# Kernel optimization log

Measured on AMD Instinct MI355X. Metric: run time of the kernel, lower is better.

Reference implementation:

```python
import jax, jax.numpy as jnp
import numpy as np

N_NODES = 65536
N_GRAPHS = 32
NODES_PER_GRAPH = 2048
N_EDGES = 1048576
F_IN, H1, H2, OUT = 16, 64, 64, 12


def gcn_conv(x, src, dst, W, b, num_nodes):
    """PyG GCNConv: out = D^{-1/2} (A+I) D^{-1/2} X W + b."""
    loop = jnp.arange(num_nodes, dtype=src.dtype)
    s = jnp.concatenate([src, loop])  # sources incl. self-loops
    d = jnp.concatenate([dst, loop])  # targets incl. self-loops
    deg = jax.ops.segment_sum(jnp.ones_like(d, dtype=x.dtype), d, num_segments=num_nodes)
    dinv = jnp.where(deg > 0, jax.lax.rsqrt(deg), 0.0)
    norm = dinv[s] * dinv[d]  # [E+N]
    h = x @ W  # [N, H]
    msg = h[s] * norm[:, None]  # [E+N, H] -- dominant memory traffic
    return jax.ops.segment_sum(msg, d, num_segments=num_nodes) + b


def setup_inputs() -> dict:
    key = jax.random.key(0)
    k = jax.random.split(key, 8)
    x = jax.random.normal(k[0], (N_NODES, F_IN), dtype=jnp.float32)
    edge_index = jax.random.randint(k[1], (2, N_EDGES), 0, N_NODES, dtype=jnp.int32)
    batch = jnp.repeat(jnp.arange(N_GRAPHS, dtype=jnp.int32), NODES_PER_GRAPH)
    s1 = 1.0 / np.sqrt(F_IN)
    s2 = 1.0 / np.sqrt(H1)
    s3 = 1.0 / np.sqrt(H2 * NODES_PER_GRAPH)
    W1 = jax.random.uniform(k[2], (F_IN, H1), jnp.float32, -s1, s1)
    b1 = jnp.zeros((H1,), jnp.float32)
    W2 = jax.random.uniform(k[3], (H1, H2), jnp.float32, -s2, s2)
    b2 = jnp.zeros((H2,), jnp.float32)
    Wfc = jax.random.uniform(k[4], (H2 * NODES_PER_GRAPH, OUT), jnp.float32, -s3, s3)
    bfc = jax.random.uniform(k[5], (OUT,), jnp.float32, -s3, s3)
    return {"x": x, "edge_index": edge_index, "batch": batch,
            "W1": W1, "b1": b1, "W2": W2, "b2": b2, "Wfc": Wfc, "bfc": bfc}


def reference(x, edge_index, batch, W1, b1, W2, b2, Wfc, bfc):
    src, dst = edge_index[0], edge_index[1]
    h = gcn_conv(x, src, dst, W1, b1, N_NODES)
    h = jnp.tanh(h)  # act1 (dropout rate 0 -> identity)
    h = gcn_conv(h, src, dst, W2, b2, N_NODES)
    h = jnp.tanh(h)  # act2
    # batch is sorted with exactly NODES_PER_GRAPH nodes per graph, so the
    # per-graph masked concat is a reshape: [G, P*H2]
    h_concat = h.reshape(N_GRAPHS, NODES_PER_GRAPH * H2)
    return h_concat @ Wfc + bfc
```

## Files before the change

### kernel.cpp

```cpp
#include <hip/hip_runtime.h>
#include <hip/hip_fp16.h>

#define N_NODES 65536
#define N_EDGES 1048576
#define F_IN    16
#define H       64
#define N_GRAPHS 32
#define NPG     2048
#define OUT_F   12
#define KPG     (NPG * H)
#define CAP     4864
#define NPB     16


__global__ __launch_bounds__(256) void init_kernel(int* __restrict__ gCursor,
                                                   const float* __restrict__ bfc,
                                                   float* __restrict__ out) {
    int t = threadIdx.x;
    gCursor[t] = t * CAP;
    for (int i = t; i < N_GRAPHS * OUT_F; i += 256) out[i] = bfc[i % OUT_F];
}

__global__ __launch_bounds__(256) void binA_kernel(const int* __restrict__ src,
                                                   const int* __restrict__ dst,
                                                   int* __restrict__ gCursor,
                                                   unsigned int* __restrict__ binned) {
    __shared__ int hist[256];
    __shared__ int sc[256];
    __shared__ int bnd[257];
    __shared__ int lcur[256];
    __shared__ int blkBase[256];
    __shared__ unsigned int staged[4096];
    int t = threadIdx.x;
    hist[t] = 0; lcur[t] = 0;
    __syncthreads();
    int e0 = blockIdx.x * 4096;
    unsigned int rec[16];
#pragma unroll
    for (int i = 0; i < 16; i++) {
        int e = e0 + i * 256 + t;
        unsigned int s = (unsigned int)src[e];
        unsigned int d = (unsigned int)dst[e];
        rec[i] = s | (d << 16);
        atomicAdd(&hist[d >> 8], 1);
    }
    __syncthreads();
    int cnt = hist[t];
    if (cnt) blkBase[t] = atomicAdd(&gCursor[t], cnt);
    sc[t] = cnt;
    __syncthreads();
    for (int off = 1; off < 256; off <<= 1) {
        int v = (t >= off) ? sc[t - off] : 0;
        __syncthreads();
        sc[t] += v;
        __syncthreads();
    }
    bnd[t] = sc[t] - cnt;
    if (t == 255) bnd[256] = 4096;
    __syncthreads();
#pragma unroll
    for (int i = 0; i < 16; i++) {
        int b = rec[i] >> 24;
        int p = bnd[b] + atomicAdd(&lcur[b], 1);
        staged[p] = rec[i];
    }
    __syncthreads();
    for (int i = t; i < 4096; i += 256) {
        int lo = 0;
#pragma unroll
        for (int s = 128; s > 0; s >>= 1)
            if (bnd[lo + s] <= i) lo += s;
        binned[blkBase[lo] + (i - bnd[lo])] = staged[i];
    }
}

__global__ __launch_bounds__(256) void binB_g1_kernel(const unsigned int* __restrict__ binned,
                                                      const int* __restrict__ gCursor,
                                                      const float* __restrict__ x,
                                                      int2* __restrict__ rowinfo,
                                                      unsigned short* __restrict__ nbr,
                                                      __half2* __restrict__ g1h) {
    __shared__ int hist[256];
    __shared__ int sc[256];
    __shared__ int off[256];
    __shared__ int cur[256];
    __shared__ unsigned short outS[8192];
    int b = blockIdx.x, t = threadIdx.x;
    int base = b * CAP;
    int cnt  = gCursor[b] - base;
    hist[t] = 0; cur[t] = 0;
    __syncthreads();
    for (int i = t; i < cnt; i += 256) {
        unsigned int r = binned[base + i];
        atomicAdd(&hist[(r >> 16) & 255], 1);
    }
    __syncthreads();
    int c = hist[t];
    sc[t] = c;
    __syncthreads();
    for (int o = 1; o < 256; o <<= 1) {
        int v = (t >= o) ? sc[t - o] : 0;
        __syncthreads();
        sc[t] += v;
        __syncthreads();
    }
    off[t] = sc[t] - c;
    int nd = (b << 8) + t;
    float dv = rsqrtf((float)(c + 1));
    rowinfo[nd] = make_int2(base + sc[t] - c, c);
    {
        const float4* xr = (const float4*)(x + (size_t)nd * F_IN);
        float4 x0 = xr[0], x1 = xr[1], x2 = xr[2], x3 = xr[3];
        __half2* gr = g1h + nd * 8;
        gr[0] = __floats2half2_rn(x0.x * dv, x0.y * dv);
        gr[1] = __floats2half2_rn(x0.z * dv, x0.w * dv);
        gr[2] = __floats2half2_rn(x1.x * dv, x1.y * dv);
        gr[3] = __floats2half2_rn(x1.z * dv, x1.w * dv);
        gr[4] = __floats2half2_rn(x2.x * dv, x2.y * dv);
        gr[5] = __floats2half2_rn(x2.z * dv, x2.w * dv);
        gr[6] = __floats2half2_rn(x3.x * dv, x3.y * dv);
        gr[7] = __floats2half2_rn(x3.z * dv, x3.w * dv);
    }
    __syncthreads();
    for (int i = t; i < cnt; i += 256) {
        unsigned int r = binned[base + i];
        int n = (r >> 16) & 255;
        int p = off[n] + atomicAdd(&cur[n], 1);
        outS[p] = (unsigned short)(r & 0xFFFF);
    }
    __syncthreads();
    for (int i = t; i < cnt; i += 256) nbr[base + i] = outS[i];
}

__device__ __forceinline__ void add8(float* acc, float4 q) {
    union { float4 f; __half2 h[4]; } u; u.f = q;
#pragma unroll
    for (int c = 0; c < 4; c++) {
        float2 p = __half22float2(u.h[c]);
        acc[2 * c]     += p.x;
        acc[2 * c + 1] += p.y;
    }
}
__device__ __forceinline__ void add4(float* acc, float2 q) {
    union { float2 f; __half2 h[2]; } u; u.f = q;
    float2 p0 = __half22float2(u.h[0]);
    float2 p1 = __half22float2(u.h[1]);
    acc[0] += p0.x; acc[1] += p0.y; acc[2] += p1.x; acc[3] += p1.y;
}

__global__ __launch_bounds__(256) void agg1_gemm1_kernel(const __half2* __restrict__ g1h,
                                                         const int2* __restrict__ rowinfo,
                                                         const unsigned short* __restrict__ nbr,
                                                         const float* __restrict__ W1,
                                                         const float* __restrict__ b1,
                                                         __half* __restrict__ g2h) {
    const float2* g1v = (const float2*)g1h;
    __shared__ float Ws[F_IN * H];
    __shared__ float bs[H];
    int t = threadIdx.x;
    for (int i = t; i < F_IN * H; i += 256) Ws[i] = W1[i];
    if (t < H) bs[t] = b1[t];
    __syncthreads();
    int lane = t & 63;
    int w    = t >> 6;
    int f4   = lane & 3;
    int sub  = lane >> 2;
    int v    = blockIdx.x * NPB + w;
    int2 ri  = rowinfo[v];
    int nb   = (int)nbr[ri.x + lane];
#pragma unroll 1
    for (int it = 0; it < NPB / 4; ++it) {
        int vc = v;
        int r0 = ri.x, er = ri.y;
        int nbc = nb;
        float2 sq = g1v[(vc << 2) + f4];
        if (it < NPB / 4 - 1) ri = rowinfo[vc + 4];
        float acc[4] = {0.f, 0.f, 0.f, 0.f};
        int j = 0;
        for (; j + 32 <= er; j += 32) {
            int u0 = __shfl(nbc, j + sub, 64);
            int u1 = __shfl(nbc, j + 16 + sub, 64);
            float2 q0 = g1v[(u0 << 2) + f4];
            float2 q1 = g1v[(u1 << 2) + f4];
            add4(acc, q0);
            add4(acc, q1);
        }
        for (; j < er && j < 64; j += 16) {
            int idx = j + sub;
            int u = __shfl(nbc, idx < er ? idx : 0, 64);
            float2 q = g1v[(u << 2) + f4];
            if (idx < er) add4(acc, q);
        }
        for (int base = 64; base < er; base += 64) {
            int nbx = (int)nbr[r0 + base + lane];
            for (int jj = 0; jj < 64 && base + jj < er; jj += 16) {
                int idx = jj + sub;
                int u = __shfl(nbx, (base + idx) < er ? idx : 0, 64);
                float2 q = g1v[(u << 2) + f4];
                if (base + idx < er) add4(acc, q);
            }
        }
        if (it < NPB / 4 - 1) nb = (int)nbr[ri.x + lane];
#pragma unroll
        for (int i = 0; i < 4; i++) {
            acc[i] += __shfl_xor(acc[i], 4, 64);
            acc[i] += __shfl_xor(acc[i], 8, 64);
            acc[i] += __shfl_xor(acc[i], 16, 64);
            acc[i] += __shfl_xor(acc[i], 32, 64);
        }
        add4(acc, sq);
        float dv = rsqrtf((float)(er + 1));
#pragma unroll
        for (int i = 0; i < 4; i++) acc[i] *= dv;
        float s = bs[lane];
#pragma unroll
        for (int k = 0; k < F_IN; ++k) {
            float bk = __shfl(acc[k & 3], k >> 2, 64);
            s += bk * Ws[k * H + lane];
        }
        g2h[(vc << 6) + lane] = __float2half(dv * tanhf(s));
        v += 4;
    }
}

__global__ __launch_bounds__(256) void agg2_kernel(const __half2* __restrict__ g2h,
                                                   const int2* __restrict__ rowinfo,
                                                   const unsigned short* __restrict__ nbr,
                                                   float* __restrict__ a2) {
    const float4* g2v = (const float4*)g2h;
    int t    = threadIdx.x;
    int lane = t & 63;
    int w    = t >> 6;
    int f8   = lane & 7;
    int sub  = lane >> 3;
    int v    = blockIdx.x * NPB + w;
    int2 ri  = rowinfo[v];
    int nb   = (int)nbr[ri.x + lane];
#pragma unroll 1
    for (int it = 0; it < NPB / 4; ++it) {
        int vc = v;
        int r0 = ri.x, er = ri.y;
        int nbc = nb;
        float4 sq = g2v[(vc << 3) + f8];
        if (it < NPB / 4 - 1) ri = rowinfo[vc + 4];
        float acc[8] = {0.f, 0.f, 0.f, 0.f, 0.f, 0.f, 0.f, 0.f};
        int j = 0;
        for (; j + 16 <= er; j += 16) {
            int u0 = __shfl(nbc, j + sub, 64);
            int u1 = __shfl(nbc, j + 8 + sub, 64);
            float4 q0 = g2v[(u0 << 3) + f8];
            float4 q1 = g2v[(u1 << 3) + f8];
            add8(acc, q0);
            add8(acc, q1);
        }
        for (; j < er && j < 64; j += 8) {
            int idx = j + sub;
            int u = __shfl(nbc, idx < er ? idx : 0, 64);
            float4 q = g2v[(u << 3) + f8];
            if (idx < er) add8(acc, q);
        }
        for (int base = 64; base < er; base += 64) {
            int nbx = (int)nbr[r0 + base + lane];
            for (int jj = 0; jj < 64 && base + jj < er; jj += 8) {
                int idx = jj + sub;
                int u = __shfl(nbx, (base + idx) < er ? idx : 0, 64);
                float4 q = g2v[(u << 3) + f8];
                if (base + idx < er) add8(acc, q);
            }
        }
        if (it < NPB / 4 - 1) nb = (int)nbr[ri.x + lane];
#pragma unroll
        for (int i = 0; i < 8; i++) {
            acc[i] += __shfl_xor(acc[i], 8, 64);
            acc[i] += __shfl_xor(acc[i], 16, 64);
            acc[i] += __shfl_xor(acc[i], 32, 64);
        }
        add8(acc, sq);
        float dv = rsqrtf((float)(er + 1));
#pragma unroll
        for (int i = 0; i < 8; i++) acc[i] *= dv;
        if (sub == 0) {
            float4* dp = (float4*)(a2 + ((size_t)vc << 6) + (f8 << 3));
            dp[0] = make_float4(acc[0], acc[1], acc[2], acc[3]);
            dp[1] = make_float4(acc[4], acc[5], acc[6], acc[7]);
        }
        v += 4;
    }
}

__global__ __launch_bounds__(256) void gemm2_fc_kernel(const float* __restrict__ a2,
                                                       const float* __restrict__ W2,
                                                       const float* __restrict__ b2,
                                                       const float* __restrict__ Wfc,
                                                       float* __restrict__ out) {
    __shared__ float Ws[H * H];
    __shared__ float As[16][H];
    __shared__ float bs[H];
    __shared__ float red[4][OUT_F];
    int t = threadIdx.x;
    for (int i = t; i < H * H; i += 256) Ws[i] = W2[i];
    if (t < H) bs[t] = b2[t];
    {
        const float4* ap = (const float4*)(a2 + ((size_t)blockIdx.x << 10));
        float4 q = ap[t];
        int node = t >> 4;
        int k    = (t & 15) << 2;
        As[node][k]     = q.x;
        As[node][k + 1] = q.y;
        As[node][k + 2] = q.z;
        As[node][k + 3] = q.w;
    }
    __syncthreads();
    int lane = t & 63, w = t >> 6;
    int v0 = blockIdx.x * 16;
    int g  = blockIdx.x >> 7;
    float pa[OUT_F];
#pragma unroll
    for (int j = 0; j < OUT_F; j++) pa[j] = 0.f;
#pragma unroll
    for (int it = 0; it < 4; ++it) {
        int nloc = (it << 2) + w;
        int v = v0 + nloc;
        const float* ar = As[nloc];
        float s = bs[lane];
#pragma unroll
        for (int k = 0; k < H; ++k) s += ar[k] * Ws[k * H + lane];
        float hv = tanhf(s);
        int vl = v & (NPG - 1);
        const float4* wr = (const float4*)(Wfc + (size_t)(vl * H + lane) * OUT_F);
        float4 w0 = wr[0], w1 = wr[1], w2 = wr[2];
        pa[0]  += hv * w0.x;  pa[1]  += hv * w0.y;
        pa[2]  += hv * w0.z;  pa[3]  += hv * w0.w;
        pa[4]  += hv * w1.x;  pa[5]  += hv * w1.y;
        pa[6]  += hv * w1.z;  pa[7]  += hv * w1.w;
        pa[8]  += hv * w2.x;  pa[9]  += hv * w2.y;
        pa[10] += hv * w2.z;  pa[11] += hv * w2.w;
    }
#pragma unroll
    for (int j = 0; j < OUT_F; j++) {
        float vv = pa[j];
        vv += __shfl_xor(vv, 1, 64);  vv += __shfl_xor(vv, 2, 64);
        vv += __shfl_xor(vv, 4, 64);  vv += __shfl_xor(vv, 8, 64);
        vv += __shfl_xor(vv, 16, 64); vv += __shfl_xor(vv, 32, 64);
        pa[j] = vv;
    }
    if (lane == 0) {
#pragma unroll
        for (int j = 0; j < OUT_F; j++) red[w][j] = pa[j];
    }
    __syncthreads();
    if (t < OUT_F)
        atomicAdd(&out[g * OUT_F + t], red[0][t] + red[1][t] + red[2][t] + red[3][t]);
}

extern "C" void kernel_launch(void* const* d_in, const int* in_sizes, int n_in,
                              void* d_out, int out_size, void* d_ws, size_t ws_size,
                              hipStream_t stream) {
    const float* x    = (const float*)d_in[0];
    const int*   edge = (const int*)d_in[1];
    const int*   src  = edge;
    const int*   dst  = edge + N_EDGES;
    const float* W1  = (const float*)d_in[3];
    const float* b1  = (const float*)d_in[4];
    const float* W2  = (const float*)d_in[5];
    const float* b2  = (const float*)d_in[6];
    const float* Wfc = (const float*)d_in[7];
    const float* bfc = (const float*)d_in[8];
    float* out = (float*)d_out;

    char* p = (char*)d_ws;
    auto alloc = [&](size_t n) { char* r = p; p += (n + 255) & ~(size_t)255; return r; };
    int*   gCursor    = (int*)alloc(256 * 4);
    int2*  rowinfo    = (int2*)alloc((size_t)N_NODES * 8);
    unsigned short* nbr = (unsigned short*)alloc((size_t)256 * CAP * 2 + 256);
    __half* g1h       = (__half*)alloc((size_t)N_NODES * F_IN * 2);
    __half* g2h       = (__half*)alloc((size_t)N_NODES * H * 2);
    float* a2         = (float*)alloc((size_t)N_NODES * H * 4);
    unsigned int* binned = (unsigned int*)alloc((size_t)256 * CAP * 4);

    init_kernel<<<1, 256, 0, stream>>>(gCursor, bfc, out);
    binA_kernel<<<256, 256, 0, stream>>>(src, dst, gCursor, binned);
    binB_g1_kernel<<<256, 256, 0, stream>>>(binned, gCursor, x, rowinfo, nbr,
                                            (__half2*)g1h);
    agg1_gemm1_kernel<<<N_NODES / NPB, 256, 0, stream>>>((const __half2*)g1h, rowinfo, nbr,
                                                         W1, b1, g2h);
    agg2_kernel<<<N_NODES / NPB, 256, 0, stream>>>((const __half2*)g2h, rowinfo, nbr, a2);
    gemm2_fc_kernel<<<N_NODES / 16, 256, 0, stream>>>(a2, W2, b2, Wfc, out);
}
```

Measured before the change: 203.1 us.

## Register-block gemm2_fc over 16 nodes per wave with 64 nodes per block

The final GEMM+FC kernel now handles 64 nodes per block instead of 16. Each wave keeps 16 node accumulators in registers and reuses every W2 value loaded from shared memory across all 16 nodes, reading A rows as float4 broadcasts. This cuts shared-memory traffic per FMA, amortizes the W2 staging across four times as many nodes, and launches a quarter of the blocks. In exchange it uses more registers and shared memory per block and has fewer blocks to fill the GPU.

```diff
diff --git a/kernel.cpp b/kernel.cpp
--- a/kernel.cpp
+++ b/kernel.cpp
@@ -294,47 +294,54 @@
                                                        const float* __restrict__ Wfc,
                                                        float* __restrict__ out) {
     __shared__ float Ws[H * H];
-    __shared__ float As[16][H];
+    __shared__ float As[64 * H];
     __shared__ float bs[H];
     __shared__ float red[4][OUT_F];
     int t = threadIdx.x;
     for (int i = t; i < H * H; i += 256) Ws[i] = W2[i];
     if (t < H) bs[t] = b2[t];
     {
-        const float4* ap = (const float4*)(a2 + ((size_t)blockIdx.x << 10));
-        float4 q = ap[t];
-        int node = t >> 4;
-        int k    = (t & 15) << 2;
-        As[node][k]     = q.x;
-        As[node][k + 1] = q.y;
-        As[node][k + 2] = q.z;
-        As[node][k + 3] = q.w;
+        const float4* ap = (const float4*)(a2 + ((size_t)blockIdx.x << 12));
+        float4* asp = (float4*)As;
+#pragma unroll
+        for (int i = 0; i < 4; i++) asp[i * 256 + t] = ap[i * 256 + t];
     }
     __syncthreads();
     int lane = t & 63, w = t >> 6;
-    int v0 = blockIdx.x * 16;
-    int g  = blockIdx.x >> 7;
+    int v0 = blockIdx.x * 64 + (w << 4);
+    int g  = blockIdx.x >> 5;
+    float acc[16];
+#pragma unroll
+    for (int j = 0; j < 16; j++) acc[j] = bs[lane];
+    const float* asBase = As + ((w << 4) * H);
+#pragma unroll 2
+    for (int kc = 0; kc < H / 4; ++kc) {
+        int k0 = kc << 2;
+        float w0 = Ws[(k0 + 0) * H + lane];
+        float w1 = Ws[(k0 + 1) * H + lane];
+        float w2 = Ws[(k0 + 2) * H + lane];
+        float w3 = Ws[(k0 + 3) * H + lane];
+#pragma unroll
+        for (int j = 0; j < 16; ++j) {
+            float4 aq = *(const float4*)(asBase + j * H + k0);
+            acc[j] += aq.x * w0 + aq.y * w1 + aq.z * w2 + aq.w * w3;
+        }
+    }
     float pa[OUT_F];
 #pragma unroll
     for (int j = 0; j < OUT_F; j++) pa[j] = 0.f;
 #pragma unroll
-    for (int it = 0; it < 4; ++it) {
-        int nloc = (it << 2) + w;
-        int v = v0 + nloc;
-        const float* ar = As[nloc];
-        float s = bs[lane];
-#pragma unroll
-        for (int k = 0; k < H; ++k) s += ar[k] * Ws[k * H + lane];
-        float hv = tanhf(s);
-        int vl = v & (NPG - 1);
+    for (int j = 0; j < 16; ++j) {
+        float hv = tanhf(acc[j]);
+        int vl = (v0 + j) & (NPG - 1);
         const float4* wr = (const float4*)(Wfc + (size_t)(vl * H + lane) * OUT_F);
-        float4 w0 = wr[0], w1 = wr[1], w2 = wr[2];
-        pa[0]  += hv * w0.x;  pa[1]  += hv * w0.y;
-        pa[2]  += hv * w0.z;  pa[3]  += hv * w0.w;
-        pa[4]  += hv * w1.x;  pa[5]  += hv * w1.y;
-        pa[6]  += hv * w1.z;  pa[7]  += hv * w1.w;
-        pa[8]  += hv * w2.x;  pa[9]  += hv * w2.y;
-        pa[10] += hv * w2.z;  pa[11] += hv * w2.w;
+        float4 q0 = wr[0], q1 = wr[1], q2 = wr[2];
+        pa[0]  += hv * q0.x;  pa[1]  += hv * q0.y;
+        pa[2]  += hv * q0.z;  pa[3]  += hv * q0.w;
+        pa[4]  += hv * q1.x;  pa[5]  += hv * q1.y;
+        pa[6]  += hv * q1.z;  pa[7]  += hv * q1.w;
+        pa[8]  += hv * q2.x;  pa[9]  += hv * q2.y;
+        pa[10] += hv * q2.z;  pa[11] += hv * q2.w;
     }
 #pragma unroll
     for (int j = 0; j < OUT_F; j++) {
@@ -385,5 +392,5 @@
     agg1_gemm1_kernel<<<N_NODES / NPB, 256, 0, stream>>>((const __half2*)g1h, rowinfo, nbr,
                                                          W1, b1, g2h);
     agg2_kernel<<<N_NODES / NPB, 256, 0, stream>>>((const __half2*)g2h, rowinfo, nbr, a2);
-    gemm2_fc_kernel<<<N_NODES / 16, 256, 0, stream>>>(a2, W2, b2, Wfc, out);
-}
+    gemm2_fc_kernel<<<N_NODES / 64, 256, 0, stream>>>(a2, W2, b2, Wfc, out);
+}
```

Measured after the change: 187.0 us. 1.09x faster.
